# Performance work log

Measured on AMD Instinct MI355X. Metric: run time of the kernel, lower is better.

The kernel has to match this reference:

```python
import jax, jax.numpy as jnp
import numpy as np

N = 100000
IN_C = 128
OUT_C = 128
E = 1600000


def setup_inputs() -> dict:
    key = jax.random.key(0)
    k1, k2, k3, k4 = jax.random.split(key, 4)
    x = jax.random.normal(k1, (N, IN_C), dtype=jnp.float32)
    edge_index = jax.random.randint(k2, (2, E), 0, N, dtype=jnp.int64)
    # GCNConv params: linear weight (stored [in, out] for x @ W) and bias [out]
    W = jax.random.normal(k3, (IN_C, OUT_C), dtype=jnp.float32) / np.sqrt(IN_C)
    b = jax.random.normal(k4, (OUT_C,), dtype=jnp.float32) * 0.01
    return {"x": x, "edge_index": edge_index, "W": W, "b": b}


def reference(x, edge_index, W, b):
    n = x.shape[0]
    # add self loops (PyG GCNConv default add_self_loops=True)
    loop = jnp.arange(n, dtype=edge_index.dtype)
    src = jnp.concatenate([edge_index[0], loop])  # message sources
    dst = jnp.concatenate([edge_index[1], loop])  # aggregation targets
    # symmetric normalization: deg over targets (edge weight 1, incl. self loops)
    deg = jax.ops.segment_sum(jnp.ones_like(dst, dtype=x.dtype), dst, num_segments=n)
    dinv = jnp.where(deg > 0, jax.lax.rsqrt(deg), 0.0)
    norm = dinv[src] * dinv[dst]  # [E+N]
    # linear transform then gather-scale-scatter aggregation
    h = x @ W  # [N, out]
    msgs = h[src] * norm[:, None]  # [E+N, out] -- dominant memory traffic
    out = jax.ops.segment_sum(msgs, dst, num_segments=n)
    return out + b
```

## Files before the change

kernel.cpp:

```cpp
#include <hip/hip_runtime.h>


#define SCAN_T 256
#define SCAN_E 1024
#define WPB 4
#define CAP 2560
#define SC_T 8192

typedef __attribute__((ext_vector_type(8))) short short8;
typedef __attribute__((ext_vector_type(4))) float f32x4;

__device__ __forceinline__ unsigned short f2bf(float f) {
  unsigned int u = __float_as_uint(f);
  u += 0x7FFFu + ((u >> 16) & 1u);
  return (unsigned short)(u >> 16);
}
__device__ __forceinline__ float bf_lo(unsigned int u) { return __uint_as_float(u << 16); }
__device__ __forceinline__ float bf_hi(unsigned int u) { return __uint_as_float(u & 0xFFFF0000u); }


__global__ void k_zero(int* __restrict__ p, int m) {
  int i = blockIdx.x * blockDim.x + threadIdx.x;
  if (i < m) p[i] = 0;
}

__global__ void __launch_bounds__(512) k_scatter(
    const int* __restrict__ ei, int* __restrict__ bcursor,
    int* __restrict__ pairs, int E, int B) {
  __shared__ int hist[1024];
  int t = threadIdx.x;
  for (int b = t; b < B; b += 512) hist[b] = 0;
  __syncthreads();
  int e0 = blockIdx.x * SC_T;
  int eend = min(e0 + SC_T, E);
  for (int e = e0 + t * 4; e < eend; e += 2048) {
    if (e + 3 < eend) {
      int4 d = *(const int4*)(ei + E + e);
      atomicAdd(&hist[((unsigned)d.x) >> 7], 1);
      atomicAdd(&hist[((unsigned)d.y) >> 7], 1);
      atomicAdd(&hist[((unsigned)d.z) >> 7], 1);
      atomicAdd(&hist[((unsigned)d.w) >> 7], 1);
    } else {
      for (int q = e; q < eend; ++q) atomicAdd(&hist[((unsigned)ei[E + q]) >> 7], 1);
    }
  }
  __syncthreads();
  for (int b = t; b < B; b += 512) {
    int c = hist[b];
    hist[b] = c ? atomicAdd(&bcursor[b], c) : 0;
  }
  __syncthreads();
  for (int e = e0 + t * 4; e < eend; e += 2048) {
    if (e + 3 < eend) {
      int4 s = *(const int4*)(ei + e);
      int4 d = *(const int4*)(ei + E + e);
      int b0 = ((unsigned)d.x) >> 7; int p0 = atomicAdd(&hist[b0], 1);
      if (p0 < CAP) pairs[(size_t)b0 * CAP + p0] = ((d.x & 127) << 17) | s.x;
      int b1 = ((unsigned)d.y) >> 7; int p1 = atomicAdd(&hist[b1], 1);
      if (p1 < CAP) pairs[(size_t)b1 * CAP + p1] = ((d.y & 127) << 17) | s.y;
      int b2 = ((unsigned)d.z) >> 7; int p2 = atomicAdd(&hist[b2], 1);
      if (p2 < CAP) pairs[(size_t)b2 * CAP + p2] = ((d.z & 127) << 17) | s.z;
      int b3 = ((unsigned)d.w) >> 7; int p3 = atomicAdd(&hist[b3], 1);
      if (p3 < CAP) pairs[(size_t)b3 * CAP + p3] = ((d.w & 127) << 17) | s.w;
    } else {
      for (int q = e; q < eend; ++q) {
        int dst = ei[E + q], src = ei[q];
        int b0 = ((unsigned)dst) >> 7; int p0 = atomicAdd(&hist[b0], 1);
        if (p0 < CAP) pairs[(size_t)b0 * CAP + p0] = ((dst & 127) << 17) | src;
      }
    }
  }
}

__global__ void __launch_bounds__(256) k_deg(
    const int* __restrict__ pairs, const int* __restrict__ bcursor,
    float* __restrict__ dinv, int n) {
  __shared__ int hist[128];
  int t = threadIdx.x;
  int b = blockIdx.x;
  if (t < 128) hist[t] = 0;
  __syncthreads();
  int cnt = min(bcursor[b], CAP);
  const int* __restrict__ gp = pairs + (size_t)b * CAP;
  for (int i = t; i < cnt; i += 256) atomicAdd(&hist[gp[i] >> 17], 1);
  __syncthreads();
  if (t < 128) {
    int node = b * 128 + t;
    if (node < n) dinv[node] = rsqrtf((float)hist[t] + 1.0f);
  }
}

__global__ void __launch_bounds__(256) k_gemm_h(
    const float* __restrict__ x, const float* __restrict__ W,
    const float* __restrict__ dinv, unsigned short* __restrict__ h, int n) {
  __shared__ alignas(16) unsigned short Wt[128][136];
  int t = threadIdx.x;
#pragma unroll
  for (int p = 0; p < 16; ++p) {
    int task = p * 256 + t;
    int kg = task >> 7, nn = task & 127;
    float w0 = W[(kg * 4 + 0) * 128 + nn];
    float w1 = W[(kg * 4 + 1) * 128 + nn];
    float w2 = W[(kg * 4 + 2) * 128 + nn];
    float w3 = W[(kg * 4 + 3) * 128 + nn];
    ushort4 u;
    u.x = f2bf(w0); u.y = f2bf(w1); u.z = f2bf(w2); u.w = f2bf(w3);
    *(ushort4*)&Wt[nn][kg * 4] = u;
  }
  __syncthreads();
  int w = t >> 6, lane = t & 63;
  int q = lane >> 4, m = lane & 15;
  int r0 = blockIdx.x * 64 + w * 16;
  f32x4 acc[8];
#pragma unroll
  for (int nt = 0; nt < 8; ++nt) acc[nt] = (f32x4){0.f, 0.f, 0.f, 0.f};
  float dscale[4];
#pragma unroll
  for (int rg = 0; rg < 4; ++rg) {
    int r = r0 + q * 4 + rg;
    dscale[rg] = dinv[r < n ? r : n - 1];
  }
#pragma unroll
  for (int ks = 0; ks < 4; ++ks) {
    int row = r0 + m;
    row = row < n ? row : n - 1;
    const float* xp = x + (size_t)row * 128 + ks * 32 + q * 8;
    float4 a0 = *(const float4*)xp;
    float4 a1 = *(const float4*)(xp + 4);
    short8 af;
    af[0] = (short)f2bf(a0.x); af[1] = (short)f2bf(a0.y);
    af[2] = (short)f2bf(a0.z); af[3] = (short)f2bf(a0.w);
    af[4] = (short)f2bf(a1.x); af[5] = (short)f2bf(a1.y);
    af[6] = (short)f2bf(a1.z); af[7] = (short)f2bf(a1.w);
#pragma unroll
    for (int nt = 0; nt < 8; ++nt) {
      short8 bf = *(const short8*)&Wt[nt * 16 + m][ks * 32 + q * 8];
      acc[nt] = __builtin_amdgcn_mfma_f32_16x16x32_bf16(af, bf, acc[nt], 0, 0, 0);
    }
  }
#pragma unroll
  for (int nt = 0; nt < 8; ++nt)
#pragma unroll
    for (int rg = 0; rg < 4; ++rg) {
      int r = r0 + q * 4 + rg;
      if (r < n) h[(size_t)r * 128 + nt * 16 + m] = f2bf(acc[nt][rg] * dscale[rg]);
    }
}

__global__ void __launch_bounds__(512) k_sort_agg(
    const int* __restrict__ pairs, const int* __restrict__ bcursor,
    const uint4* __restrict__ h4, const float* __restrict__ bias,
    float* __restrict__ out, int n) {
  __shared__ int pb[CAP];
  __shared__ int sorted[CAP];
  __shared__ int hist[128], base_[128], cur[128];
  __shared__ int nextn;
  int t = threadIdx.x;
  int b = blockIdx.x;
  if (t < 128) { hist[t] = 0; cur[t] = 0; }
  if (t == 0) nextn = 0;
  __syncthreads();
  int cnt = min(bcursor[b], CAP);
  const int* __restrict__ gp = pairs + (size_t)b * CAP;
  for (int i = t; i < cnt; i += 512) {
    int p = gp[i];
    pb[i] = p;
    atomicAdd(&hist[p >> 17], 1);
  }
  __syncthreads();
  if (t < 128) base_[t] = hist[t];
  __syncthreads();
#pragma unroll
  for (int d = 1; d < 128; d <<= 1) {
    int v = (t < 128 && t >= d) ? base_[t - d] : 0;
    __syncthreads();
    if (t < 128) base_[t] += v;
    __syncthreads();
  }
  if (t < 128) base_[t] -= hist[t];
  __syncthreads();
  for (int i = t; i < cnt; i += 512) {
    int p = pb[i];
    int d = p >> 17;
    int pos = base_[d] + atomicAdd(&cur[d], 1);
    sorted[pos] = p & 0x1FFFF;
  }
  __syncthreads();

  int lane = t & 63;
  int ln = lane & 15;
  int nbase = b << 7;
  for (;;) {
    int row = 0;
    if (ln == 0) row = atomicAdd(&nextn, 1);
    row = __shfl(row, lane & 48, 64);
    if (row >= 128) break;
    int node = nbase + row;
    bool act = node < n;
    uint4 sp = make_uint4(0u, 0u, 0u, 0u);
    if (act) sp = h4[(size_t)node * 16 + ln];
    float a[8];
    a[0] = bf_lo(sp.x); a[1] = bf_hi(sp.x);
    a[2] = bf_lo(sp.y); a[3] = bf_hi(sp.y);
    a[4] = bf_lo(sp.z); a[5] = bf_hi(sp.z);
    a[6] = bf_lo(sp.w); a[7] = bf_hi(sp.w);
    int s = base_[row];
    int cd = hist[row];
    int end = s + cd;
    for (; s + 8 <= end; s += 8) {
      uint4 u[8];
#pragma unroll
      for (int k = 0; k < 8; ++k) {
        int idx = sorted[s + k];
        u[k] = h4[(size_t)idx * 16 + ln];
      }
#pragma unroll
      for (int k = 0; k < 8; ++k) {
        a[0] += bf_lo(u[k].x); a[1] += bf_hi(u[k].x);
        a[2] += bf_lo(u[k].y); a[3] += bf_hi(u[k].y);
        a[4] += bf_lo(u[k].z); a[5] += bf_hi(u[k].z);
        a[6] += bf_lo(u[k].w); a[7] += bf_hi(u[k].w);
      }
    }
    for (; s + 4 <= end; s += 4) {
      uint4 u[4];
#pragma unroll
      for (int k = 0; k < 4; ++k) {
        int idx = sorted[s + k];
        u[k] = h4[(size_t)idx * 16 + ln];
      }
#pragma unroll
      for (int k = 0; k < 4; ++k) {
        a[0] += bf_lo(u[k].x); a[1] += bf_hi(u[k].x);
        a[2] += bf_lo(u[k].y); a[3] += bf_hi(u[k].y);
        a[4] += bf_lo(u[k].z); a[5] += bf_hi(u[k].z);
        a[6] += bf_lo(u[k].w); a[7] += bf_hi(u[k].w);
      }
    }
    for (; s < end; ++s) {
      int idx = sorted[s];
      uint4 u = h4[(size_t)idx * 16 + ln];
      a[0] += bf_lo(u.x); a[1] += bf_hi(u.x);
      a[2] += bf_lo(u.y); a[3] += bf_hi(u.y);
      a[4] += bf_lo(u.z); a[5] += bf_hi(u.z);
      a[6] += bf_lo(u.w); a[7] += bf_hi(u.w);
    }
    if (act) {
      float di = rsqrtf((float)cd + 1.0f);
      float4 b0 = ((const float4*)bias)[2 * ln];
      float4 b1 = ((const float4*)bias)[2 * ln + 1];
      f32x4 r0, r1;
      r0[0] = fmaf(a[0], di, b0.x); r0[1] = fmaf(a[1], di, b0.y);
      r0[2] = fmaf(a[2], di, b0.z); r0[3] = fmaf(a[3], di, b0.w);
      r1[0] = fmaf(a[4], di, b1.x); r1[1] = fmaf(a[5], di, b1.y);
      r1[2] = fmaf(a[6], di, b1.z); r1[3] = fmaf(a[7], di, b1.w);
      f32x4* op = (f32x4*)(out + (size_t)node * 128 + ln * 8);
      __builtin_nontemporal_store(r0, op);
      __builtin_nontemporal_store(r1, op + 1);
    }
  }
}


__global__ void k_init(int* __restrict__ cnt, int n) {
  int i = blockIdx.x * blockDim.x + threadIdx.x;
  if (i < n) cnt[i] = 0;
}

__global__ void k_count4(const int* __restrict__ ei, int* __restrict__ cnt, int E) {
  int i = blockIdx.x * blockDim.x + threadIdx.x;
  int e = i * 4;
  if (e + 3 < E) {
    int4 d = *(const int4*)(ei + E + e);
    atomicAdd(&cnt[d.x], 1); atomicAdd(&cnt[d.y], 1);
    atomicAdd(&cnt[d.z], 1); atomicAdd(&cnt[d.w], 1);
  } else {
    for (; e < E; ++e) atomicAdd(&cnt[ei[E + e]], 1);
  }
}

__global__ void k_scan_local(const int* __restrict__ cnt, int* __restrict__ offs,
                             int* __restrict__ bsums, int n) {
  __shared__ int sh[SCAN_T];
  int t = threadIdx.x;
  int base = blockIdx.x * SCAN_E + t * 4;
  int v0 = 0, v1 = 0, v2 = 0, v3 = 0;
  if (base + 0 < n) v0 = cnt[base + 0];
  if (base + 1 < n) v1 = cnt[base + 1];
  if (base + 2 < n) v2 = cnt[base + 2];
  if (base + 3 < n) v3 = cnt[base + 3];
  int sum = v0 + v1 + v2 + v3;
  sh[t] = sum;
  __syncthreads();
  for (int d = 1; d < SCAN_T; d <<= 1) {
    int xv = (t >= d) ? sh[t - d] : 0;
    __syncthreads();
    sh[t] += xv;
    __syncthreads();
  }
  int run = sh[t] - sum;
  if (base + 0 < n) offs[base + 0] = run; run += v0;
  if (base + 1 < n) offs[base + 1] = run; run += v1;
  if (base + 2 < n) offs[base + 2] = run; run += v2;
  if (base + 3 < n) offs[base + 3] = run;
  if (t == SCAN_T - 1) bsums[blockIdx.x] = sh[t];
}

__global__ void k_scan_bsums(int* __restrict__ bsums, int nb) {
  __shared__ int sh[SCAN_T];
  int t = threadIdx.x;
  int v = (t < nb) ? bsums[t] : 0;
  sh[t] = v;
  __syncthreads();
  for (int d = 1; d < SCAN_T; d <<= 1) {
    int xv = (t >= d) ? sh[t - d] : 0;
    __syncthreads();
    sh[t] += xv;
    __syncthreads();
  }
  if (t < nb) bsums[t] = sh[t] - v;
}

__global__ void k_scan_finish(int* __restrict__ offs, const int* __restrict__ bsums,
                              const int* __restrict__ cnt, int* __restrict__ offs2,
                              float* __restrict__ dinv, int n) {
  int i = blockIdx.x * blockDim.x + threadIdx.x;
  if (i < n) {
    int o = offs[i] + bsums[i / SCAN_E];
    offs[i] = o;
    offs2[i] = o;
    dinv[i] = rsqrtf((float)cnt[i] + 1.0f);
  }
}

__global__ void k_fill4(const int* __restrict__ ei, int* __restrict__ offs2,
                        int* __restrict__ csr, int E) {
  int i = blockIdx.x * blockDim.x + threadIdx.x;
  int e = i * 4;
  if (e + 3 < E) {
    int4 s = *(const int4*)(ei + e);
    int4 d = *(const int4*)(ei + E + e);
    csr[atomicAdd(&offs2[d.x], 1)] = s.x;
    csr[atomicAdd(&offs2[d.y], 1)] = s.y;
    csr[atomicAdd(&offs2[d.z], 1)] = s.z;
    csr[atomicAdd(&offs2[d.w], 1)] = s.w;
  } else {
    for (; e < E; ++e) csr[atomicAdd(&offs2[ei[E + e]], 1)] = ei[e];
  }
}

__global__ void __launch_bounds__(256) k_agg_bias_csr(
    const unsigned int* __restrict__ h2, const float* __restrict__ dinv,
    const int* __restrict__ offs, const int* __restrict__ cnt,
    const int* __restrict__ csr, const float* __restrict__ bias,
    float* __restrict__ out, int n) {
  int node = blockIdx.x * WPB + (threadIdx.x >> 6);
  int lane = threadIdx.x & 63;
  if (node >= n) return;
  unsigned int sp = h2[(size_t)node * 64 + lane];
  float ax = bf_lo(sp), ay = bf_hi(sp);
  int s = offs[node];
  int end = s + cnt[node];
  for (; s + 8 <= end; s += 8) {
    int i0 = csr[s + 0], i1 = csr[s + 1], i2 = csr[s + 2], i3 = csr[s + 3];
    int i4 = csr[s + 4], i5 = csr[s + 5], i6 = csr[s + 6], i7 = csr[s + 7];
    unsigned int u0 = h2[(size_t)i0 * 64 + lane];
    unsigned int u1 = h2[(size_t)i1 * 64 + lane];
    unsigned int u2 = h2[(size_t)i2 * 64 + lane];
    unsigned int u3 = h2[(size_t)i3 * 64 + lane];
    unsigned int u4 = h2[(size_t)i4 * 64 + lane];
    unsigned int u5 = h2[(size_t)i5 * 64 + lane];
    unsigned int u6 = h2[(size_t)i6 * 64 + lane];
    unsigned int u7 = h2[(size_t)i7 * 64 + lane];
    ax += (bf_lo(u0) + bf_lo(u1)) + (bf_lo(u2) + bf_lo(u3)) +
          (bf_lo(u4) + bf_lo(u5)) + (bf_lo(u6) + bf_lo(u7));
    ay += (bf_hi(u0) + bf_hi(u1)) + (bf_hi(u2) + bf_hi(u3)) +
          (bf_hi(u4) + bf_hi(u5)) + (bf_hi(u6) + bf_hi(u7));
  }
  for (; s < end; ++s) {
    unsigned int u = h2[(size_t)csr[s] * 64 + lane];
    ax += bf_lo(u); ay += bf_hi(u);
  }
  float di = dinv[node];
  float2 bb = ((const float2*)bias)[lane];
  float2 r;
  r.x = fmaf(ax, di, bb.x);
  r.y = fmaf(ay, di, bb.y);
  ((float2*)out)[(size_t)node * 64 + lane] = r;
}

extern "C" void kernel_launch(void* const* d_in, const int* in_sizes, int n_in,
                              void* d_out, int out_size, void* d_ws, size_t ws_size,
                              hipStream_t stream) {
  const float* x = (const float*)d_in[0];
  const int* ei = (const int*)d_in[1];
  const float* Wm = (const float*)d_in[2];
  const float* bias = (const float*)d_in[3];
  float* out = (float*)d_out;

  int N = in_sizes[0] / 128;
  int E = in_sizes[1] / 2;
  int NB64 = (N + 63) >> 6;
  int NB128 = (N + 127) >> 7;

  int nb_n = (N + 255) / 256;
  int nb_e4 = ((E + 3) / 4 + 255) / 256;

  size_t off_bc = ((size_t)N * 4 + 255) & ~(size_t)255;
  size_t off_pairs = off_bc + 4096;
  size_t off_h = (off_pairs + (size_t)NB128 * CAP * 4 + 255) & ~(size_t)255;
  size_t need13 = off_h + (size_t)N * 256;

  if (ws_size >= need13 && N <= (1 << 17) && NB128 <= 1024) {
    char* p = (char*)d_ws;
    float* dinv = (float*)p;
    int* bcursor = (int*)(p + off_bc);
    int* pairs = (int*)(p + off_pairs);
    unsigned short* h = (unsigned short*)(p + off_h);

    k_zero<<<4, 256, 0, stream>>>(bcursor, 1024);
    k_scatter<<<(E + SC_T - 1) / SC_T, 512, 0, stream>>>(ei, bcursor, pairs, E, NB128);
    k_deg<<<NB128, 256, 0, stream>>>(pairs, bcursor, dinv, N);
    k_gemm_h<<<NB64, 256, 0, stream>>>(x, Wm, dinv, h, N);
    k_sort_agg<<<NB128, 512, 0, stream>>>(pairs, bcursor, (const uint4*)h, bias, out, N);
    return;
  }

  char* p = (char*)d_ws;
  int* cnt = (int*)p;        p += (size_t)N * 4;
  int* offs = (int*)p;       p += (size_t)N * 4;
  int* offs2 = (int*)p;      p += (size_t)N * 4;
  float* dinv = (float*)p;   p += (size_t)N * 4;
  int* bsums = (int*)p;      p += 1024;
  int* csr = (int*)p;        p += (size_t)E * 4;
  unsigned short* h = (unsigned short*)p;

  int nb_scan = (N + SCAN_E - 1) / SCAN_E;

  k_init<<<nb_n, 256, 0, stream>>>(cnt, N);
  k_count4<<<nb_e4, 256, 0, stream>>>(ei, cnt, E);
  k_scan_local<<<nb_scan, SCAN_T, 0, stream>>>(cnt, offs, bsums, N);
  k_scan_bsums<<<1, SCAN_T, 0, stream>>>(bsums, nb_scan);
  k_scan_finish<<<nb_n, 256, 0, stream>>>(offs, bsums, cnt, offs2, dinv, N);
  k_fill4<<<nb_e4, 256, 0, stream>>>(ei, offs2, csr, E);
  k_gemm_h<<<NB64, 256, 0, stream>>>(x, Wm, dinv, h, N);
  k_agg_bias_csr<<<(N + WPB - 1) / WPB, 256, 0, stream>>>(
      (const unsigned int*)h, dinv, offs, cnt, csr, bias, out, N);
}
```

Baseline: 205.4 us.

## Fuse degree histogram into GEMM kernel and drop pair staging buffer

Merges the per-bucket degree counting kernel into the GEMM kernel. Each block now handles 128 rows, builds the degree histogram in shared memory and computes the rsqrt scale inline, so the dinv array and one launch go away. In the sort/aggregate kernel, the shared pb staging buffer is removed and pairs are read twice from global memory instead, which cuts shared memory use and may allow more blocks per CU. The trade-off is half as many GEMM blocks, each doing twice the work, plus a second global read of the pairs.

Measured after the change: 204.3 us. Within noise of the previous version (-0.5%).

```diff
diff --git a/kernel.cpp b/kernel.cpp
--- a/kernel.cpp
+++ b/kernel.cpp
@@ -72,9 +72,11 @@
   }
 }
 
-__global__ void __launch_bounds__(256) k_deg(
+__global__ void __launch_bounds__(256) k_gemm_hd(
+    const float* __restrict__ x, const float* __restrict__ W,
     const int* __restrict__ pairs, const int* __restrict__ bcursor,
-    float* __restrict__ dinv, int n) {
+    unsigned short* __restrict__ h, int n) {
+  __shared__ alignas(16) unsigned short Wt[128][136];
   __shared__ int hist[128];
   int t = threadIdx.x;
   int b = blockIdx.x;
@@ -83,18 +85,6 @@
   int cnt = min(bcursor[b], CAP);
   const int* __restrict__ gp = pairs + (size_t)b * CAP;
   for (int i = t; i < cnt; i += 256) atomicAdd(&hist[gp[i] >> 17], 1);
-  __syncthreads();
-  if (t < 128) {
-    int node = b * 128 + t;
-    if (node < n) dinv[node] = rsqrtf((float)hist[t] + 1.0f);
-  }
-}
-
-__global__ void __launch_bounds__(256) k_gemm_h(
-    const float* __restrict__ x, const float* __restrict__ W,
-    const float* __restrict__ dinv, unsigned short* __restrict__ h, int n) {
-  __shared__ alignas(16) unsigned short Wt[128][136];
-  int t = threadIdx.x;
 #pragma unroll
   for (int p = 0; p < 16; ++p) {
     int task = p * 256 + t;
@@ -110,48 +100,49 @@
   __syncthreads();
   int w = t >> 6, lane = t & 63;
   int q = lane >> 4, m = lane & 15;
-  int r0 = blockIdx.x * 64 + w * 16;
-  f32x4 acc[8];
-#pragma unroll
-  for (int nt = 0; nt < 8; ++nt) acc[nt] = (f32x4){0.f, 0.f, 0.f, 0.f};
-  float dscale[4];
-#pragma unroll
-  for (int rg = 0; rg < 4; ++rg) {
-    int r = r0 + q * 4 + rg;
-    dscale[rg] = dinv[r < n ? r : n - 1];
-  }
-#pragma unroll
-  for (int ks = 0; ks < 4; ++ks) {
-    int row = r0 + m;
-    row = row < n ? row : n - 1;
-    const float* xp = x + (size_t)row * 128 + ks * 32 + q * 8;
-    float4 a0 = *(const float4*)xp;
-    float4 a1 = *(const float4*)(xp + 4);
-    short8 af;
-    af[0] = (short)f2bf(a0.x); af[1] = (short)f2bf(a0.y);
-    af[2] = (short)f2bf(a0.z); af[3] = (short)f2bf(a0.w);
-    af[4] = (short)f2bf(a1.x); af[5] = (short)f2bf(a1.y);
-    af[6] = (short)f2bf(a1.z); af[7] = (short)f2bf(a1.w);
-#pragma unroll
-    for (int nt = 0; nt < 8; ++nt) {
-      short8 bf = *(const short8*)&Wt[nt * 16 + m][ks * 32 + q * 8];
-      acc[nt] = __builtin_amdgcn_mfma_f32_16x16x32_bf16(af, bf, acc[nt], 0, 0, 0);
-    }
-  }
-#pragma unroll
-  for (int nt = 0; nt < 8; ++nt)
-#pragma unroll
-    for (int rg = 0; rg < 4; ++rg) {
-      int r = r0 + q * 4 + rg;
-      if (r < n) h[(size_t)r * 128 + nt * 16 + m] = f2bf(acc[nt][rg] * dscale[rg]);
-    }
+#pragma unroll
+  for (int rep = 0; rep < 2; ++rep) {
+    int lbase = rep * 64 + w * 16;
+    int r0 = (b << 7) + lbase;
+    f32x4 acc[8];
+#pragma unroll
+    for (int nt = 0; nt < 8; ++nt) acc[nt] = (f32x4){0.f, 0.f, 0.f, 0.f};
+    float dscale[4];
+#pragma unroll
+    for (int rg = 0; rg < 4; ++rg)
+      dscale[rg] = rsqrtf((float)hist[lbase + q * 4 + rg] + 1.0f);
+#pragma unroll
+    for (int ks = 0; ks < 4; ++ks) {
+      int row = r0 + m;
+      row = row < n ? row : n - 1;
+      const float* xp = x + (size_t)row * 128 + ks * 32 + q * 8;
+      float4 a0 = *(const float4*)xp;
+      float4 a1 = *(const float4*)(xp + 4);
+      short8 af;
+      af[0] = (short)f2bf(a0.x); af[1] = (short)f2bf(a0.y);
+      af[2] = (short)f2bf(a0.z); af[3] = (short)f2bf(a0.w);
+      af[4] = (short)f2bf(a1.x); af[5] = (short)f2bf(a1.y);
+      af[6] = (short)f2bf(a1.z); af[7] = (short)f2bf(a1.w);
+#pragma unroll
+      for (int nt = 0; nt < 8; ++nt) {
+        short8 bf = *(const short8*)&Wt[nt * 16 + m][ks * 32 + q * 8];
+        acc[nt] = __builtin_amdgcn_mfma_f32_16x16x32_bf16(af, bf, acc[nt], 0, 0, 0);
+      }
+    }
+#pragma unroll
+    for (int nt = 0; nt < 8; ++nt)
+#pragma unroll
+      for (int rg = 0; rg < 4; ++rg) {
+        int r = r0 + q * 4 + rg;
+        if (r < n) h[(size_t)r * 128 + nt * 16 + m] = f2bf(acc[nt][rg] * dscale[rg]);
+      }
+  }
 }
 
 __global__ void __launch_bounds__(512) k_sort_agg(
     const int* __restrict__ pairs, const int* __restrict__ bcursor,
     const uint4* __restrict__ h4, const float* __restrict__ bias,
     float* __restrict__ out, int n) {
-  __shared__ int pb[CAP];
   __shared__ int sorted[CAP];
   __shared__ int hist[128], base_[128], cur[128];
   __shared__ int nextn;
@@ -162,25 +153,21 @@
   __syncthreads();
   int cnt = min(bcursor[b], CAP);
   const int* __restrict__ gp = pairs + (size_t)b * CAP;
+  for (int i = t; i < cnt; i += 512) atomicAdd(&hist[gp[i] >> 17], 1);
+  __syncthreads();
+  if (t < 128) base_[t] = hist[t];
+  __syncthreads();
+#pragma unroll
+  for (int d = 1; d < 128; d <<= 1) {
+    int v = (t < 128 && t >= d) ? base_[t - d] : 0;
+    __syncthreads();
+    if (t < 128) base_[t] += v;
+    __syncthreads();
+  }
+  if (t < 128) base_[t] -= hist[t];
+  __syncthreads();
   for (int i = t; i < cnt; i += 512) {
     int p = gp[i];
-    pb[i] = p;
-    atomicAdd(&hist[p >> 17], 1);
-  }
-  __syncthreads();
-  if (t < 128) base_[t] = hist[t];
-  __syncthreads();
-#pragma unroll
-  for (int d = 1; d < 128; d <<= 1) {
-    int v = (t < 128 && t >= d) ? base_[t - d] : 0;
-    __syncthreads();
-    if (t < 128) base_[t] += v;
-    __syncthreads();
-  }
-  if (t < 128) base_[t] -= hist[t];
-  __syncthreads();
-  for (int i = t; i < cnt; i += 512) {
-    int p = pb[i];
     int d = p >> 17;
     int pos = base_[d] + atomicAdd(&cur[d], 1);
     sorted[pos] = p & 0x1FFFF;
@@ -347,6 +334,63 @@
   } else {
     for (; e < E; ++e) csr[atomicAdd(&offs2[ei[E + e]], 1)] = ei[e];
   }
+}
+
+__global__ void __launch_bounds__(256) k_gemm_h(
+    const float* __restrict__ x, const float* __restrict__ W,
+    const float* __restrict__ dinv, unsigned short* __restrict__ h, int n) {
+  __shared__ alignas(16) unsigned short Wt[128][136];
+  int t = threadIdx.x;
+#pragma unroll
+  for (int p = 0; p < 16; ++p) {
+    int task = p * 256 + t;
+    int kg = task >> 7, nn = task & 127;
+    float w0 = W[(kg * 4 + 0) * 128 + nn];
+    float w1 = W[(kg * 4 + 1) * 128 + nn];
+    float w2 = W[(kg * 4 + 2) * 128 + nn];
+    float w3 = W[(kg * 4 + 3) * 128 + nn];
+    ushort4 u;
+    u.x = f2bf(w0); u.y = f2bf(w1); u.z = f2bf(w2); u.w = f2bf(w3);
+    *(ushort4*)&Wt[nn][kg * 4] = u;
+  }
+  __syncthreads();
+  int w = t >> 6, lane = t & 63;
+  int q = lane >> 4, m = lane & 15;
+  int r0 = blockIdx.x * 64 + w * 16;
+  f32x4 acc[8];
+#pragma unroll
+  for (int nt = 0; nt < 8; ++nt) acc[nt] = (f32x4){0.f, 0.f, 0.f, 0.f};
+  float dscale[4];
+#pragma unroll
+  for (int rg = 0; rg < 4; ++rg) {
+    int r = r0 + q * 4 + rg;
+    dscale[rg] = dinv[r < n ? r : n - 1];
+  }
+#pragma unroll
+  for (int ks = 0; ks < 4; ++ks) {
+    int row = r0 + m;
+    row = row < n ? row : n - 1;
+    const float* xp = x + (size_t)row * 128 + ks * 32 + q * 8;
+    float4 a0 = *(const float4*)xp;
+    float4 a1 = *(const float4*)(xp + 4);
+    short8 af;
+    af[0] = (short)f2bf(a0.x); af[1] = (short)f2bf(a0.y);
+    af[2] = (short)f2bf(a0.z); af[3] = (short)f2bf(a0.w);
+    af[4] = (short)f2bf(a1.x); af[5] = (short)f2bf(a1.y);
+    af[6] = (short)f2bf(a1.z); af[7] = (short)f2bf(a1.w);
+#pragma unroll
+    for (int nt = 0; nt < 8; ++nt) {
+      short8 bf = *(const short8*)&Wt[nt * 16 + m][ks * 32 + q * 8];
+      acc[nt] = __builtin_amdgcn_mfma_f32_16x16x32_bf16(af, bf, acc[nt], 0, 0, 0);
+    }
+  }
+#pragma unroll
+  for (int nt = 0; nt < 8; ++nt)
+#pragma unroll
+    for (int rg = 0; rg < 4; ++rg) {
+      int r = r0 + q * 4 + rg;
+      if (r < n) h[(size_t)r * 128 + nt * 16 + m] = f2bf(acc[nt][rg] * dscale[rg]);
+    }
 }
 
 __global__ void __launch_bounds__(256) k_agg_bias_csr(
@@ -406,22 +450,19 @@
   int nb_n = (N + 255) / 256;
   int nb_e4 = ((E + 3) / 4 + 255) / 256;
 
-  size_t off_bc = ((size_t)N * 4 + 255) & ~(size_t)255;
-  size_t off_pairs = off_bc + 4096;
+  size_t off_pairs = 4096;
   size_t off_h = (off_pairs + (size_t)NB128 * CAP * 4 + 255) & ~(size_t)255;
-  size_t need13 = off_h + (size_t)N * 256;
-
-  if (ws_size >= need13 && N <= (1 << 17) && NB128 <= 1024) {
+  size_t need14 = off_h + (size_t)N * 256;
+
+  if (ws_size >= need14 && N <= (1 << 17) && NB128 <= 1024) {
     char* p = (char*)d_ws;
-    float* dinv = (float*)p;
-    int* bcursor = (int*)(p + off_bc);
+    int* bcursor = (int*)p;
     int* pairs = (int*)(p + off_pairs);
     unsigned short* h = (unsigned short*)(p + off_h);
 
     k_zero<<<4, 256, 0, stream>>>(bcursor, 1024);
     k_scatter<<<(E + SC_T - 1) / SC_T, 512, 0, stream>>>(ei, bcursor, pairs, E, NB128);
-    k_deg<<<NB128, 256, 0, stream>>>(pairs, bcursor, dinv, N);
-    k_gemm_h<<<NB64, 256, 0, stream>>>(x, Wm, dinv, h, N);
+    k_gemm_hd<<<NB128, 256, 0, stream>>>(x, Wm, pairs, bcursor, h, N);
     k_sort_agg<<<NB128, 512, 0, stream>>>(pairs, bcursor, (const uint4*)h, bias, out, N);
     return;
   }
```
